# Kernel optimization log

Hardware: AMD Instinct MI355X
Metric: run time of the kernel (lower is better)

Reference implementation:

```python
import jax, jax.numpy as jnp
import numpy as np

IN_CH = 512
MID_CH = IN_CH // 8  # 64


def setup_inputs() -> dict:
    key = jax.random.key(0)
    ks = jax.random.split(key, 7)
    B, C, H, W = 8, IN_CH, 64, 64
    s = 1.0 / np.sqrt(C)
    x = jax.random.normal(ks[0], (B, C, H, W), dtype=jnp.float32)
    wq = jax.random.normal(ks[1], (MID_CH, C), dtype=jnp.float32) * s
    bq = jax.random.normal(ks[2], (MID_CH,), dtype=jnp.float32) * 0.01
    wk = jax.random.normal(ks[3], (MID_CH, C), dtype=jnp.float32) * s
    bk = jax.random.normal(ks[4], (MID_CH,), dtype=jnp.float32) * 0.01
    wv = jax.random.normal(ks[5], (C, C), dtype=jnp.float32) * s
    bv = jax.random.normal(ks[6], (C,), dtype=jnp.float32) * 0.01
    gamma = jnp.array([0.5], dtype=jnp.float32)
    return {"x": x, "wq": wq, "bq": bq, "wk": wk, "bk": bk,
            "wv": wv, "bv": bv, "gamma": gamma}


def reference(x, wq, bq, wk, bk, wv, bv, gamma):
    B, C, H, W = x.shape
    N = H * W
    xf = x.reshape(B, C, N)  # flatten spatial -> [B, C, N]
    # 1x1 convs are channel-wise matmuls
    q = jnp.einsum('mc,bcn->bnm', wq, xf) + bq  # [B, N, mid]
    k = jnp.einsum('mc,bcn->bmn', wk, xf) + bk[None, :, None]  # [B, mid, N]
    v = jnp.einsum('oc,bcn->bon', wv, xf) + bv[None, :, None]  # [B, C, N]
    sim = jnp.einsum('bnm,bmj->bnj', q, k)  # [B, N, N]
    sim = jax.nn.softmax(sim, axis=-1)
    # feat[b,c,i] = sum_j v[b,c,j] * sim[b,i,j]   (value @ sim^T)
    feat = jnp.einsum('bcj,bij->bci', v, sim).reshape(B, C, H, W)
    return gamma[0] * feat + x
```

## Files before the change

kernel.cpp:

```cpp
#include <hip/hip_runtime.h>
#include <hip/hip_bf16.h>


#define BB 8
#define CC 512
#define MM 64
#define NN 4096
#define LOG2E 1.4426950408889634f

typedef __attribute__((ext_vector_type(8))) short bf16x8;
typedef __attribute__((ext_vector_type(8))) _Float16 f16x8;
typedef __attribute__((ext_vector_type(4))) float f32x4;
typedef __attribute__((ext_vector_type(16))) float f32x16;

__device__ unsigned g_kmax[BB];

__device__ __forceinline__ unsigned short f2bf(float f) {
  union { float f; unsigned u; } v; v.f = f;
  unsigned r = v.u + 0x7fffu + ((v.u >> 16) & 1u);
  return (unsigned short)(r >> 16);
}
__device__ __forceinline__ float bf2f(unsigned short h) {
  union { unsigned u; float f; } v; v.u = ((unsigned)h) << 16;
  return v.f;
}
__device__ __forceinline__ unsigned short f2h(float f) {
  union { _Float16 h; unsigned short u; } v; v.h = (_Float16)f;
  return v.u;
}

#define PC_BARRIER()                                        \
  do {                                                      \
    __builtin_amdgcn_sched_barrier(0);                      \
    asm volatile("s_waitcnt lgkmcnt(0)" ::: "memory");      \
    __builtin_amdgcn_s_barrier();                           \
    __builtin_amdgcn_sched_barrier(0);                      \
  } while (0)

__global__ __launch_bounds__(256) void k_wconv(
    const float* __restrict__ wq, const float* __restrict__ wk,
    const float* __restrict__ wv,
    unsigned short* __restrict__ wqhi, unsigned short* __restrict__ wqlo,
    unsigned short* __restrict__ wkhi, unsigned short* __restrict__ wklo,
    unsigned short* __restrict__ wvbf) {
  const int tid = blockIdx.x * 256 + threadIdx.x;
  if (tid < BB) g_kmax[tid] = 0u;
  if (tid < MM * CC) {
    float v = wq[tid];
    unsigned short h = f2bf(v);
    wqhi[tid] = h; wqlo[tid] = f2bf(v - bf2f(h));
    v = wk[tid]; h = f2bf(v);
    wkhi[tid] = h; wklo[tid] = f2bf(v - bf2f(h));
  }
  for (int i = tid; i < CC * CC; i += 65536) wvbf[i] = f2bf(wv[i]);
}

__global__ __launch_bounds__(256) void k_transpose(const float* __restrict__ x,
                                                   unsigned short* __restrict__ xT) {
  __shared__ float tile[64][65];
  const int b = blockIdx.z, c0 = blockIdx.y * 64, n0 = blockIdx.x * 64;
  const int t = threadIdx.x;
  {
    const int nq = (t & 15) * 4, cl0 = t >> 4;
    const float* xp = x + ((size_t)b * CC + c0) * NN + n0;
#pragma unroll
    for (int r = 0; r < 4; r++) {
      const int row = cl0 + r * 16;
      const f32x4 v = *reinterpret_cast<const f32x4*>(xp + (size_t)row * NN + nq);
      tile[row][nq] = v[0]; tile[row][nq + 1] = v[1];
      tile[row][nq + 2] = v[2]; tile[row][nq + 3] = v[3];
    }
  }
  __syncthreads();
  {
    const int cq = (t & 15) * 4, nl0 = t >> 4;
    unsigned short* xtp = xT + ((size_t)b * NN + n0) * CC + c0;
#pragma unroll
    for (int r = 0; r < 4; r++) {
      const int n = nl0 + r * 16;
      const ushort4 o = make_ushort4(f2bf(tile[cq][n]), f2bf(tile[cq + 1][n]),
                                     f2bf(tile[cq + 2][n]), f2bf(tile[cq + 3][n]));
      *reinterpret_cast<ushort4*>(xtp + (size_t)n * CC + cq) = o;
    }
  }
}

__global__ __launch_bounds__(256, 2) void k_proj(
    const unsigned short* __restrict__ xT,
    const unsigned short* __restrict__ wqhi, const unsigned short* __restrict__ wqlo,
    const unsigned short* __restrict__ wkhi, const unsigned short* __restrict__ wklo,
    const float* __restrict__ bq, const float* __restrict__ bk,
    const unsigned short* __restrict__ wvbf, const float* __restrict__ bv,
    unsigned short* __restrict__ qf, unsigned short* __restrict__ kf,
    unsigned short* __restrict__ vbf) {
  __shared__ float ksl[4][4][16];
  const int t = threadIdx.x, w = t >> 6, l = t & 63, lr = l & 15, g = l >> 4;

  if (blockIdx.x < 512) {
    const int b = blockIdx.x & 7;
    const int n0 = (blockIdx.x >> 3) * 64;
    const unsigned short* qhp = wqhi + (size_t)(w * 16 + lr) * CC + g * 8;
    const unsigned short* qlp = wqlo + (size_t)(w * 16 + lr) * CC + g * 8;
    const unsigned short* khp = wkhi + (size_t)(w * 16 + lr) * CC + g * 8;
    const unsigned short* klp = wklo + (size_t)(w * 16 + lr) * CC + g * 8;
    const unsigned short* xp = xT + ((size_t)b * NN + n0 + lr) * CC + g * 8;
    f32x4 qacc[4], kacc[4];
#pragma unroll
    for (int nf = 0; nf < 4; nf++) {
      qacc[nf] = f32x4{0.f, 0.f, 0.f, 0.f};
      kacc[nf] = f32x4{0.f, 0.f, 0.f, 0.f};
    }
    for (int cc = 0; cc < CC; cc += 32) {
      const bf16x8 qh8 = *reinterpret_cast<const bf16x8*>(qhp + cc);
      const bf16x8 ql8 = *reinterpret_cast<const bf16x8*>(qlp + cc);
      const bf16x8 kh8 = *reinterpret_cast<const bf16x8*>(khp + cc);
      const bf16x8 kl8 = *reinterpret_cast<const bf16x8*>(klp + cc);
      bf16x8 xb[4];
#pragma unroll
      for (int nf = 0; nf < 4; nf++)
        xb[nf] = *reinterpret_cast<const bf16x8*>(xp + (size_t)nf * 16 * CC + cc);
#pragma unroll
      for (int nf = 0; nf < 4; nf++) {
        qacc[nf] = __builtin_amdgcn_mfma_f32_16x16x32_bf16(qh8, xb[nf], qacc[nf], 0, 0, 0);
        qacc[nf] = __builtin_amdgcn_mfma_f32_16x16x32_bf16(ql8, xb[nf], qacc[nf], 0, 0, 0);
        kacc[nf] = __builtin_amdgcn_mfma_f32_16x16x32_bf16(kh8, xb[nf], kacc[nf], 0, 0, 0);
        kacc[nf] = __builtin_amdgcn_mfma_f32_16x16x32_bf16(kl8, xb[nf], kacc[nf], 0, 0, 0);
      }
    }
    float bqv[4], bkv[4];
#pragma unroll
    for (int r = 0; r < 4; r++) {
      bqv[r] = bq[w * 16 + g * 4 + r];
      bkv[r] = bk[w * 16 + g * 4 + r];
    }
    float kssp[4];
#pragma unroll
    for (int nf = 0; nf < 4; nf++) {
      float ks2 = 0.f;
      unsigned short qh[4], kh[4];
#pragma unroll
      for (int r = 0; r < 4; r++) {
        const float qv = (qacc[nf][r] + bqv[r]) * LOG2E;
        const float kv = kacc[nf][r] + bkv[r];
        qh[r] = f2h(qv); kh[r] = f2h(kv);
        ks2 += kv * kv;
      }
      kssp[nf] = ks2;
      const int n = n0 + nf * 16 + lr;
      const size_t base = ((size_t)b * NN + n) * MM + w * 16 + g * 4;
      *reinterpret_cast<ushort4*>(qf + base) = make_ushort4(qh[0], qh[1], qh[2], qh[3]);
      *reinterpret_cast<ushort4*>(kf + base) = make_ushort4(kh[0], kh[1], kh[2], kh[3]);
    }
#pragma unroll
    for (int nf = 0; nf < 4; nf++) {
      kssp[nf] += __shfl_xor(kssp[nf], 16);
      kssp[nf] += __shfl_xor(kssp[nf], 32);
    }
    if (l < 16) {
#pragma unroll
      for (int nf = 0; nf < 4; nf++) ksl[w][nf][lr] = kssp[nf];
    }
    __syncthreads();
    if (t < 64) {
      const int nf2 = t >> 4, lr2 = t & 15;
      float kn2 = ksl[0][nf2][lr2] + ksl[1][nf2][lr2] + ksl[2][nf2][lr2] + ksl[3][nf2][lr2];
#pragma unroll
      for (int d = 1; d < 64; d <<= 1) kn2 = fmaxf(kn2, __shfl_xor(kn2, d));
      if (t == 0) atomicMax(&g_kmax[b], __float_as_uint(kn2));
    }
  } else {
    const int blk = blockIdx.x - 512;
    const int b = blk >> 7, c0 = ((blk >> 4) & 7) * 64, n0 = (blk & 15) * 256;
    const int nbase = n0 + w * 64;
    f32x4 acc[4][4];
#pragma unroll
    for (int cf = 0; cf < 4; cf++)
#pragma unroll
      for (int nf = 0; nf < 4; nf++) acc[cf][nf] = f32x4{0.f, 0.f, 0.f, 0.f};
    for (int ks = 0; ks < 16; ks++) {
      const int kk = ks * 32 + g * 8;
      bf16x8 bfr[4];
#pragma unroll
      for (int nf = 0; nf < 4; nf++) {
        const int n = nbase + nf * 16 + lr;
        bfr[nf] = *reinterpret_cast<const bf16x8*>(xT + ((size_t)b * NN + n) * CC + kk);
      }
#pragma unroll
      for (int cf = 0; cf < 4; cf++) {
        const bf16x8 af = *reinterpret_cast<const bf16x8*>(
            wvbf + (size_t)(c0 + cf * 16 + lr) * CC + kk);
#pragma unroll
        for (int nf = 0; nf < 4; nf++)
          acc[cf][nf] = __builtin_amdgcn_mfma_f32_16x16x32_bf16(af, bfr[nf], acc[cf][nf], 0, 0, 0);
      }
    }
#pragma unroll
    for (int cf = 0; cf < 4; cf++) {
#pragma unroll
      for (int r = 0; r < 4; r++) {
        const int c = c0 + cf * 16 + g * 4 + r;
        const float bvv = bv[c];
#pragma unroll
        for (int nf = 0; nf < 4; nf++) {
          const int n = nbase + nf * 16 + lr;
          vbf[((size_t)b * CC + c) * NN + n] = f2bf(acc[cf][nf][r] + bvv);
        }
      }
    }
  }
}

__global__ __launch_bounds__(512, 2) void k_attn(
    const unsigned short* __restrict__ qf, const unsigned short* __restrict__ kf,
    const unsigned short* __restrict__ vbf, const float* __restrict__ x,
    const float* __restrict__ gamma, float* __restrict__ out) {
  __shared__ unsigned Pg[2][32][128];
  __shared__ float l_red[2][4][32];
  const int b = blockIdx.x & 7;
  const int i0 = (blockIdx.x >> 3) * 128;
  const int t = threadIdx.x, w = t >> 6, l = t & 63;
  const int l31 = l & 31, h = l >> 5, h4 = h * 4, h8 = h * 8;
  const int jf = w & 1;
  const int ifq = w >> 1;
  const int wc = w * 64;

  f16x8 qF[4];
#pragma unroll
  for (int kfi = 0; kfi < 4; kfi++)
    qF[kfi] = *reinterpret_cast<const f16x8*>(
        qf + ((size_t)b * NN + i0 + ifq * 32 + l31) * MM + kfi * 16 + h8);
  float mhat;
  {
    float ssq = 0.f;
#pragma unroll
    for (int kfi = 0; kfi < 4; kfi++)
#pragma unroll
      for (int e = 0; e < 8; e++) {
        const float qv = (float)qF[kfi][e];
        ssq += qv * qv;
      }
    ssq += __shfl_xor(ssq, 32);
    mhat = sqrtf(ssq) * sqrtf(__uint_as_float(g_kmax[b])) * 1.001f - 63.4786f;
  }

  const unsigned short* kp = kf + ((size_t)b * NN + jf * 32 + l31) * MM + h8;
  const unsigned short* pvp = vbf + ((size_t)b * CC + wc + l31) * NN + h8;

  f32x16 acc[2][4];
#pragma unroll
  for (int cf = 0; cf < 2; cf++)
#pragma unroll
    for (int f = 0; f < 4; f++)
      acc[cf][f] = f32x16{0.f, 0.f, 0.f, 0.f, 0.f, 0.f, 0.f, 0.f,
                          0.f, 0.f, 0.f, 0.f, 0.f, 0.f, 0.f, 0.f};
  float lsum = 0.f;

  unsigned* const pg0 = &Pg[0][0][0];
  auto produce = [&](const f16x8 (&kk)[4], int par, bool addl) {
    f32x16 sa = f32x16{0.f, 0.f, 0.f, 0.f, 0.f, 0.f, 0.f, 0.f,
                       0.f, 0.f, 0.f, 0.f, 0.f, 0.f, 0.f, 0.f};
#pragma unroll
    for (int kfi = 0; kfi < 4; kfi++)
      sa = __builtin_amdgcn_mfma_f32_32x32x16_f16(kk[kfi], qF[kfi], sa, 0, 0, 0);
    float p[16];
#pragma unroll
    for (int r = 0; r < 16; r++) p[r] = __builtin_amdgcn_exp2f(sa[r] - mhat);
    if (addl) {
      float ps = 0.f;
#pragma unroll
      for (int r = 0; r < 16; r++) ps += p[r];
      lsum += ps;
    }
    unsigned* pw = pg0 + par * (32 * 128);
#pragma unroll
    for (int s = 0; s < 8; s++) {
      unsigned u;
      asm volatile("v_cvt_pk_bf16_f32 %0, %1, %2" : "=v"(u) : "v"(p[2 * s]), "v"(p[2 * s + 1]));
      pw[(jf * 16 + (s & 1) + 4 * (s >> 1) + 2 * h) * 128 + ifq * 32 + l31] = u;
    }
  };

  f16x8 kA[4], kB[4];
#pragma unroll
  for (int kfi = 0; kfi < 4; kfi++) {
    kA[kfi] = *reinterpret_cast<const f16x8*>(kp + (size_t)kfi * 16);
    kB[kfi] = *reinterpret_cast<const f16x8*>(kp + (size_t)64 * MM + kfi * 16);
  }
  produce(kA, 0, true);
  PC_BARRIER();

  auto region = [&](int tt, f16x8 (&kuse)[4], f16x8 (&kpre)[4]) {
    const int jb = tt * 64;
    const int j2 = (jb + 128) & (NN - 1);
    const int par = tt & 1;
    bf16x8 vr[2][4];
#pragma unroll
    for (int cf = 0; cf < 2; cf++)
#pragma unroll
      for (int ks = 0; ks < 4; ks++)
        vr[cf][ks] = *reinterpret_cast<const bf16x8*>(
            pvp + (size_t)cf * (32 * NN) + jb + ks * 16);
#pragma unroll
    for (int kfi = 0; kfi < 4; kfi++)
      kpre[kfi] = *reinterpret_cast<const f16x8*>(kp + (size_t)j2 * MM + kfi * 16);
    produce(kuse, par ^ 1, jb + 64 < NN);
    const unsigned* pr = pg0 + par * (32 * 128);
    __builtin_amdgcn_s_setprio(1);
#pragma unroll
    for (int ks = 0; ks < 4; ks++) {
#pragma unroll
      for (int f = 0; f < 4; f++) {
        uint4 bw;
        bw.x = pr[(ks * 8 + h4 + 0) * 128 + f * 32 + l31];
        bw.y = pr[(ks * 8 + h4 + 1) * 128 + f * 32 + l31];
        bw.z = pr[(ks * 8 + h4 + 2) * 128 + f * 32 + l31];
        bw.w = pr[(ks * 8 + h4 + 3) * 128 + f * 32 + l31];
        const bf16x8 B = *reinterpret_cast<const bf16x8*>(&bw);
        acc[0][f] = __builtin_amdgcn_mfma_f32_32x32x16_bf16(vr[0][ks], B, acc[0][f], 0, 0, 0);
        acc[1][f] = __builtin_amdgcn_mfma_f32_32x32x16_bf16(vr[1][ks], B, acc[1][f], 0, 0, 0);
      }
    }
    __builtin_amdgcn_s_setprio(0);
    PC_BARRIER();
  };

  for (int tt = 0; tt < 32; tt++) {
    region(2 * tt, kB, kA);
    region(2 * tt + 1, kA, kB);
  }

  lsum += __shfl_xor(lsum, 32);
  if (l < 32) l_red[jf][ifq][l] = lsum;
  __syncthreads();
  const float gm = gamma[0];
  float inv[4];
#pragma unroll
  for (int f = 0; f < 4; f++)
    inv[f] = gm / (l_red[0][f][l31] + l_red[1][f][l31]);

#pragma unroll
  for (int cf = 0; cf < 2; cf++) {
#pragma unroll
    for (int f = 0; f < 4; f++) {
#pragma unroll
      for (int r = 0; r < 16; r++) {
        const int c = wc + cf * 32 + (r & 3) + 8 * (r >> 2) + 4 * h;
        const int i = i0 + f * 32 + l31;
        const size_t o = ((size_t)b * CC + c) * NN + i;
        out[o] = acc[cf][f][r] * inv[f] + x[o];
      }
    }
  }
}

extern "C" void kernel_launch(void* const* d_in, const int* in_sizes, int n_in,
                              void* d_out, int out_size, void* d_ws, size_t ws_size,
                              hipStream_t stream) {
  const float* x = (const float*)d_in[0];
  const float* wq = (const float*)d_in[1];
  const float* bq = (const float*)d_in[2];
  const float* wk = (const float*)d_in[3];
  const float* bk = (const float*)d_in[4];
  const float* wv = (const float*)d_in[5];
  const float* bv = (const float*)d_in[6];
  const float* gamma = (const float*)d_in[7];
  float* out = (float*)d_out;

  char* ws = (char*)d_ws;
  unsigned short* xT = (unsigned short*)(ws);
  unsigned short* vbf = (unsigned short*)(ws + 33554432);
  unsigned short* qfp = (unsigned short*)(ws + 67108864);
  unsigned short* kfp = (unsigned short*)(ws + 71303168);
  unsigned short* wqhi = (unsigned short*)(ws + 75497472);
  unsigned short* wqlo = (unsigned short*)(ws + 75563008);
  unsigned short* wkhi = (unsigned short*)(ws + 75628544);
  unsigned short* wklo = (unsigned short*)(ws + 75694080);
  unsigned short* wvbf = (unsigned short*)(ws + 75759616);

  k_wconv<<<256, 256, 0, stream>>>(wq, wk, wv, wqhi, wqlo, wkhi, wklo, wvbf);
  k_transpose<<<dim3(64, 8, 8), 256, 0, stream>>>(x, xT);
  k_proj<<<1536, 256, 0, stream>>>(xT, wqhi, wqlo, wkhi, wklo, bq, bk, wvbf, bv,
                                   qfp, kfp, vbf);
  k_attn<<<dim3(256), 512, 0, stream>>>(qfp, kfp, vbf, x, gamma, out);
}
```

Before: 327.9 us.

## Split attention channels across two blocks, interleave softmax with PV MFMAs

The attention kernel now launches twice as many blocks, each handling half of the 512 output channels, so every wave keeps one 32-channel accumulator set instead of two. This roughly halves accumulator registers and raises parallelism, at the cost of recomputing QK^T scores and softmax once per channel half. The V tile for the next step is prefetched, and the score exp/convert work is placed between the two halves of the PV MFMA loop to overlap with it. The P shared-memory layout changes to allow vectorized uint2 writes and uint4 reads, and the projection kernel's block index order is changed to interleave batches.

```diff
diff --git a/kernel.cpp b/kernel.cpp
--- a/kernel.cpp
+++ b/kernel.cpp
@@ -170,7 +170,10 @@
     }
   } else {
     const int blk = blockIdx.x - 512;
-    const int b = blk >> 7, c0 = ((blk >> 4) & 7) * 64, n0 = (blk & 15) * 256;
+    const int b = blk & 7;
+    const int rest = blk >> 3;
+    const int c0 = (rest & 7) * 64;
+    const int n0 = (rest >> 3) * 256;
     const int nbase = n0 + w * 64;
     f32x4 acc[4][4];
 #pragma unroll
@@ -214,15 +217,17 @@
     const unsigned short* __restrict__ qf, const unsigned short* __restrict__ kf,
     const unsigned short* __restrict__ vbf, const float* __restrict__ x,
     const float* __restrict__ gamma, float* __restrict__ out) {
-  __shared__ unsigned Pg[2][32][128];
+  __shared__ unsigned Pg[2][8][128][4];
   __shared__ float l_red[2][4][32];
   const int b = blockIdx.x & 7;
-  const int i0 = (blockIdx.x >> 3) * 128;
+  const int idx = blockIdx.x >> 3;
+  const int i0 = (idx >> 1) * 128;
+  const int ch = idx & 1;
   const int t = threadIdx.x, w = t >> 6, l = t & 63;
-  const int l31 = l & 31, h = l >> 5, h4 = h * 4, h8 = h * 8;
+  const int l31 = l & 31, h = l >> 5, h8 = h * 8;
   const int jf = w & 1;
   const int ifq = w >> 1;
-  const int wc = w * 64;
+  const int wc = ch * 256 + w * 32;
 
   f16x8 qF[4];
 #pragma unroll
@@ -246,39 +251,14 @@
   const unsigned short* kp = kf + ((size_t)b * NN + jf * 32 + l31) * MM + h8;
   const unsigned short* pvp = vbf + ((size_t)b * CC + wc + l31) * NN + h8;
 
-  f32x16 acc[2][4];
-#pragma unroll
-  for (int cf = 0; cf < 2; cf++)
-#pragma unroll
-    for (int f = 0; f < 4; f++)
-      acc[cf][f] = f32x16{0.f, 0.f, 0.f, 0.f, 0.f, 0.f, 0.f, 0.f,
-                          0.f, 0.f, 0.f, 0.f, 0.f, 0.f, 0.f, 0.f};
+  f32x16 acc[4];
+#pragma unroll
+  for (int f = 0; f < 4; f++)
+    acc[f] = f32x16{0.f, 0.f, 0.f, 0.f, 0.f, 0.f, 0.f, 0.f,
+                    0.f, 0.f, 0.f, 0.f, 0.f, 0.f, 0.f, 0.f};
   float lsum = 0.f;
 
-  unsigned* const pg0 = &Pg[0][0][0];
-  auto produce = [&](const f16x8 (&kk)[4], int par, bool addl) {
-    f32x16 sa = f32x16{0.f, 0.f, 0.f, 0.f, 0.f, 0.f, 0.f, 0.f,
-                       0.f, 0.f, 0.f, 0.f, 0.f, 0.f, 0.f, 0.f};
-#pragma unroll
-    for (int kfi = 0; kfi < 4; kfi++)
-      sa = __builtin_amdgcn_mfma_f32_32x32x16_f16(kk[kfi], qF[kfi], sa, 0, 0, 0);
-    float p[16];
-#pragma unroll
-    for (int r = 0; r < 16; r++) p[r] = __builtin_amdgcn_exp2f(sa[r] - mhat);
-    if (addl) {
-      float ps = 0.f;
-#pragma unroll
-      for (int r = 0; r < 16; r++) ps += p[r];
-      lsum += ps;
-    }
-    unsigned* pw = pg0 + par * (32 * 128);
-#pragma unroll
-    for (int s = 0; s < 8; s++) {
-      unsigned u;
-      asm volatile("v_cvt_pk_bf16_f32 %0, %1, %2" : "=v"(u) : "v"(p[2 * s]), "v"(p[2 * s + 1]));
-      pw[(jf * 16 + (s & 1) + 4 * (s >> 1) + 2 * h) * 128 + ifq * 32 + l31] = u;
-    }
-  };
+  unsigned* const pg0 = &Pg[0][0][0][0];
 
   f16x8 kA[4], kB[4];
 #pragma unroll
@@ -286,38 +266,91 @@
     kA[kfi] = *reinterpret_cast<const f16x8*>(kp + (size_t)kfi * 16);
     kB[kfi] = *reinterpret_cast<const f16x8*>(kp + (size_t)64 * MM + kfi * 16);
   }
-  produce(kA, 0, true);
+  bf16x8 va[4], vb[4];
+#pragma unroll
+  for (int ks = 0; ks < 4; ks++)
+    va[ks] = *reinterpret_cast<const bf16x8*>(pvp + ks * 16);
+  {
+    f32x16 sa = f32x16{0.f, 0.f, 0.f, 0.f, 0.f, 0.f, 0.f, 0.f,
+                       0.f, 0.f, 0.f, 0.f, 0.f, 0.f, 0.f, 0.f};
+#pragma unroll
+    for (int kfi = 0; kfi < 4; kfi++)
+      sa = __builtin_amdgcn_mfma_f32_32x32x16_f16(kA[kfi], qF[kfi], sa, 0, 0, 0);
+    float p[16];
+#pragma unroll
+    for (int r = 0; r < 16; r++) p[r] = __builtin_amdgcn_exp2f(sa[r] - mhat);
+#pragma unroll
+    for (int r = 0; r < 16; r++) lsum += p[r];
+#pragma unroll
+    for (int k = 0; k < 4; k++) {
+      unsigned u0, u1;
+      asm volatile("v_cvt_pk_bf16_f32 %0, %1, %2" : "=v"(u0) : "v"(p[4 * k]), "v"(p[4 * k + 1]));
+      asm volatile("v_cvt_pk_bf16_f32 %0, %1, %2" : "=v"(u1) : "v"(p[4 * k + 2]), "v"(p[4 * k + 3]));
+      *reinterpret_cast<uint2*>(pg0 + ((jf * 4 + k) * 128 + ifq * 32 + l31) * 4 + 2 * h) =
+          make_uint2(u0, u1);
+    }
+  }
   PC_BARRIER();
 
-  auto region = [&](int tt, f16x8 (&kuse)[4], f16x8 (&kpre)[4]) {
+  auto region = [&](int tt, bf16x8 (&vcur)[4], bf16x8 (&vnext)[4],
+                    f16x8 (&kuse)[4], f16x8 (&kpre)[4]) {
     const int jb = tt * 64;
+    const int par = tt & 1;
+    const int j1 = (jb + 64) & (NN - 1);
     const int j2 = (jb + 128) & (NN - 1);
-    const int par = tt & 1;
-    bf16x8 vr[2][4];
-#pragma unroll
-    for (int cf = 0; cf < 2; cf++)
-#pragma unroll
-      for (int ks = 0; ks < 4; ks++)
-        vr[cf][ks] = *reinterpret_cast<const bf16x8*>(
-            pvp + (size_t)cf * (32 * NN) + jb + ks * 16);
+#pragma unroll
+    for (int ks = 0; ks < 4; ks++)
+      vnext[ks] = *reinterpret_cast<const bf16x8*>(pvp + (size_t)j1 + ks * 16);
+    f32x16 sa = f32x16{0.f, 0.f, 0.f, 0.f, 0.f, 0.f, 0.f, 0.f,
+                       0.f, 0.f, 0.f, 0.f, 0.f, 0.f, 0.f, 0.f};
+#pragma unroll
+    for (int kfi = 0; kfi < 4; kfi++)
+      sa = __builtin_amdgcn_mfma_f32_32x32x16_f16(kuse[kfi], qF[kfi], sa, 0, 0, 0);
 #pragma unroll
     for (int kfi = 0; kfi < 4; kfi++)
       kpre[kfi] = *reinterpret_cast<const f16x8*>(kp + (size_t)j2 * MM + kfi * 16);
-    produce(kuse, par ^ 1, jb + 64 < NN);
-    const unsigned* pr = pg0 + par * (32 * 128);
+    const unsigned* pr = pg0 + (par << 12);
     __builtin_amdgcn_s_setprio(1);
 #pragma unroll
-    for (int ks = 0; ks < 4; ks++) {
+    for (int ks = 0; ks < 2; ks++) {
 #pragma unroll
       for (int f = 0; f < 4; f++) {
-        uint4 bw;
-        bw.x = pr[(ks * 8 + h4 + 0) * 128 + f * 32 + l31];
-        bw.y = pr[(ks * 8 + h4 + 1) * 128 + f * 32 + l31];
-        bw.z = pr[(ks * 8 + h4 + 2) * 128 + f * 32 + l31];
-        bw.w = pr[(ks * 8 + h4 + 3) * 128 + f * 32 + l31];
+        const uint4 bw = *reinterpret_cast<const uint4*>(
+            pr + ((ks * 2 + h) * 128 + f * 32 + l31) * 4);
         const bf16x8 B = *reinterpret_cast<const bf16x8*>(&bw);
-        acc[0][f] = __builtin_amdgcn_mfma_f32_32x32x16_bf16(vr[0][ks], B, acc[0][f], 0, 0, 0);
-        acc[1][f] = __builtin_amdgcn_mfma_f32_32x32x16_bf16(vr[1][ks], B, acc[1][f], 0, 0, 0);
+        acc[f] = __builtin_amdgcn_mfma_f32_32x32x16_bf16(vcur[ks], B, acc[f], 0, 0, 0);
+      }
+    }
+    __builtin_amdgcn_s_setprio(0);
+    {
+      float p[16];
+#pragma unroll
+      for (int r = 0; r < 16; r++) p[r] = __builtin_amdgcn_exp2f(sa[r] - mhat);
+      if (jb + 64 < NN) {
+        float ps = 0.f;
+#pragma unroll
+        for (int r = 0; r < 16; r++) ps += p[r];
+        lsum += ps;
+      }
+      unsigned* pw = pg0 + ((par ^ 1) << 12);
+#pragma unroll
+      for (int k = 0; k < 4; k++) {
+        unsigned u0, u1;
+        asm volatile("v_cvt_pk_bf16_f32 %0, %1, %2" : "=v"(u0) : "v"(p[4 * k]), "v"(p[4 * k + 1]));
+        asm volatile("v_cvt_pk_bf16_f32 %0, %1, %2" : "=v"(u1) : "v"(p[4 * k + 2]), "v"(p[4 * k + 3]));
+        *reinterpret_cast<uint2*>(pw + ((jf * 4 + k) * 128 + ifq * 32 + l31) * 4 + 2 * h) =
+            make_uint2(u0, u1);
+      }
+    }
+    __builtin_amdgcn_s_setprio(1);
+#pragma unroll
+    for (int ks = 2; ks < 4; ks++) {
+#pragma unroll
+      for (int f = 0; f < 4; f++) {
+        const uint4 bw = *reinterpret_cast<const uint4*>(
+            pr + ((ks * 2 + h) * 128 + f * 32 + l31) * 4);
+        const bf16x8 B = *reinterpret_cast<const bf16x8*>(&bw);
+        acc[f] = __builtin_amdgcn_mfma_f32_32x32x16_bf16(vcur[ks], B, acc[f], 0, 0, 0);
       }
     }
     __builtin_amdgcn_s_setprio(0);
@@ -325,8 +358,8 @@
   };
 
   for (int tt = 0; tt < 32; tt++) {
-    region(2 * tt, kB, kA);
-    region(2 * tt + 1, kA, kB);
+    region(2 * tt, va, vb, kB, kA);
+    region(2 * tt + 1, vb, va, kA, kB);
   }
 
   lsum += __shfl_xor(lsum, 32);
@@ -339,16 +372,13 @@
     inv[f] = gm / (l_red[0][f][l31] + l_red[1][f][l31]);
 
 #pragma unroll
-  for (int cf = 0; cf < 2; cf++) {
-#pragma unroll
-    for (int f = 0; f < 4; f++) {
-#pragma unroll
-      for (int r = 0; r < 16; r++) {
-        const int c = wc + cf * 32 + (r & 3) + 8 * (r >> 2) + 4 * h;
-        const int i = i0 + f * 32 + l31;
-        const size_t o = ((size_t)b * CC + c) * NN + i;
-        out[o] = acc[cf][f][r] * inv[f] + x[o];
-      }
+  for (int f = 0; f < 4; f++) {
+#pragma unroll
+    for (int r = 0; r < 16; r++) {
+      const int c = wc + (r & 3) + 8 * (r >> 2) + 4 * h;
+      const int i = i0 + f * 32 + l31;
+      const size_t o = ((size_t)b * CC + c) * NN + i;
+      out[o] = acc[f][r] * inv[f] + x[o];
     }
   }
 }
@@ -381,5 +411,5 @@
   k_transpose<<<dim3(64, 8, 8), 256, 0, stream>>>(x, xT);
   k_proj<<<1536, 256, 0, stream>>>(xT, wqhi, wqlo, wkhi, wklo, bq, bk, wvbf, bv,
                                    qfp, kfp, vbf);
-  k_attn<<<dim3(256), 512, 0, stream>>>(qfp, kfp, vbf, x, gamma, out);
-}
+  k_attn<<<dim3(512), 512, 0, stream>>>(qfp, kfp, vbf, x, gamma, out);
+}
```

Measured after the change: 368.4 us. 12.3% more time.
